# Performance work log

Measured on AMD Instinct MI355X. Metric: run time of the kernel, lower is better.

The kernel has to match this reference:

```python
import jax, jax.numpy as jnp
import numpy as np

H = 16  # num_heads


def setup_inputs() -> dict:
    key = jax.random.key(0)
    ks = jax.random.split(key, 8)
    B, N, C = 16, 4096, 512
    hd = C // H
    sc = lambda k, shape: jax.random.normal(k, shape, jnp.float32) * 0.02
    return {
        "x": jax.random.normal(ks[0], (B, N, C), jnp.float32),
        "Wqkv": sc(ks[1], (C, 3 * C)),
        "bqkv": sc(ks[2], (3 * C,)),
        "pos_enc": jnp.zeros((1, N, C), jnp.float32),
        "dwc_w": sc(ks[3], (hd, 1, 5, 5)),  # OIHW, depthwise: groups = hd
        "dwc_b": sc(ks[4], (hd,)),
        "Wproj": sc(ks[5], (C, C)),
        "bproj": sc(ks[6], (C,)),
    }


def reference(x, Wqkv, bqkv, pos_enc, dwc_w, dwc_b, Wproj, bproj):
    B, N, C = x.shape
    hd = C // H
    # qkv projection
    qkv = x @ Wqkv + bqkv                       # (B, N, 3C)
    q, k, v = jnp.split(qkv, 3, axis=-1)
    k = k + pos_enc
    q = jax.nn.relu(q)
    k = jax.nn.relu(k)

    def heads(t):  # (B, N, C) -> (B*H, N, hd), fp32 as in the torch autocast-off block
        return t.reshape(B, N, H, hd).transpose(0, 2, 1, 3).reshape(B * H, N, hd).astype(jnp.float32)

    q, k, v = heads(q), heads(k), heads(v)
    # normalization z_i = 1 / (q_i . sum_j k_j + eps)
    z = 1.0 / (jnp.einsum('bic,bc->bi', q, k.sum(axis=1)) + 1e-6)   # (B*H, N)
    # kv-first path: i*j*(c+d) > c*d*(i+j) for N=4096, hd=32
    kv = jnp.einsum('bjc,bjd->bcd', k, v)                           # (B*H, hd, hd)
    out = jnp.einsum('bic,bcd->bid', q, kv) * z[..., None]          # (B*H, N, hd)
    # depthwise 5x5 conv on v reshaped to a square feature map
    w = int(N ** 0.5)
    fm = v.transpose(0, 2, 1).reshape(B * H, hd, w, w)
    fm = jax.lax.conv_general_dilated(
        fm, dwc_w, window_strides=(1, 1), padding=[(2, 2), (2, 2)],
        dimension_numbers=('NCHW', 'OIHW', 'NCHW'), feature_group_count=hd)
    fm = fm + dwc_b[None, :, None, None]
    fm = fm.reshape(B * H, hd, N).transpose(0, 2, 1)
    out = out + fm
    # merge heads and project
    out = out.reshape(B, H, N, hd).transpose(0, 2, 1, 3).reshape(B, N, C)
    return out @ Wproj + bproj
```

## Files before the change

### kernel.cpp

```cpp
#include <hip/hip_runtime.h>
#include <stdint.h>

typedef short bf16x8 __attribute__((ext_vector_type(8)));
typedef float f32x4 __attribute__((ext_vector_type(4)));
typedef unsigned short u16x8 __attribute__((ext_vector_type(8)));

__device__ __forceinline__ unsigned short f2bf(float f){
  uint32_t u = __builtin_bit_cast(uint32_t, f);
  u += 0x7FFFu + ((u >> 16) & 1u);
  return (unsigned short)(u >> 16);
}
__device__ __forceinline__ float bf2f(unsigned short h){
  uint32_t u = ((uint32_t)h) << 16;
  return __builtin_bit_cast(float, u);
}
__device__ __forceinline__ float bflo(uint32_t dw){
  return __builtin_bit_cast(float, dw << 16);
}
__device__ __forceinline__ float bfhi(uint32_t dw){
  return __builtin_bit_cast(float, dw & 0xffff0000u);
}

__device__ __forceinline__ void gload_lds16(const void* g, void* l){
  __builtin_amdgcn_global_load_lds(
      (const __attribute__((address_space(1))) uint32_t*)(g),
      (__attribute__((address_space(3))) uint32_t*)(l),
      16, 0, 0);
}

__global__ __launch_bounds__(256) void convert_x_k(const float* __restrict__ x,
                                                   unsigned short* __restrict__ xb){
  size_t i = (size_t)blockIdx.x * 256 + threadIdx.x;
  const float4* p = (const float4*)x + i * 2;
  float4 a = p[0], b = p[1];
  u16x8 o;
  o[0] = f2bf(a.x); o[1] = f2bf(a.y); o[2] = f2bf(a.z); o[3] = f2bf(a.w);
  o[4] = f2bf(b.x); o[5] = f2bf(b.y); o[6] = f2bf(b.z); o[7] = f2bf(b.w);
  *(u16x8*)(xb + i * 8) = o;
}

__global__ __launch_bounds__(256) void transpose_w_k(const float* __restrict__ Wqkv,
                                                     const float* __restrict__ Wproj,
                                                     unsigned short* __restrict__ Wqkvt,
                                                     unsigned short* __restrict__ Wprojt){
  __shared__ unsigned short t[64][68];
  int bid = blockIdx.x;
  const float* src; unsigned short* dst; int c0, j0, sstride, dstride;
  if (bid < 192){
    src = Wqkv;  dst = Wqkvt;  sstride = 1536; dstride = 512;
    c0 = (bid / 24) * 64;  j0 = (bid % 24) * 64;
  } else {
    int e = bid - 192;
    src = Wproj; dst = Wprojt; sstride = 512;  dstride = 512;
    c0 = (e >> 3) * 64;    j0 = (e & 7) * 64;
  }
  int tid = threadIdx.x;
  int rl = tid >> 6;
  int cl = tid & 63;
  #pragma unroll
  for (int i = 0; i < 16; ++i){
    int cr = i * 4 + rl;
    t[cl][cr] = f2bf(src[(size_t)(c0 + cr) * sstride + j0 + cl]);
  }
  __syncthreads();
  #pragma unroll
  for (int i = 0; i < 16; ++i){
    int jr = i * 4 + rl;
    dst[(size_t)(j0 + jr) * dstride + c0 + cl] = t[jr][cl];
  }
}

template<int EPI>
__device__ __forceinline__ void gemm_body(
    const unsigned short* __restrict__ A,
    const unsigned short* __restrict__ Bt,
    const float* __restrict__ bias,
    const float* __restrict__ pos_enc,
    unsigned short* __restrict__ oq,
    unsigned short* __restrict__ ok,
    unsigned short* __restrict__ ov,
    float* __restrict__ op,
    int NTN)
{
  __shared__ unsigned short As[2][256 * 64];
  __shared__ unsigned short Bs[2][256 * 64];
  int tid = threadIdx.x, lane = tid & 63, wid = tid >> 6;
  int nwg = gridDim.x;
  int b0 = blockIdx.x;
  int cpx = nwg >> 3;
  int swz = (b0 & 7) * cpx + (b0 >> 3);
  int tm = swz / NTN, tn = swz - tm * NTN;
  int row0 = tm << 8, col0 = tn << 8;
  int wrow = wid >> 2, wcol = wid & 3;

  f32x4 acc[8][4];
  #pragma unroll
  for (int m = 0; m < 8; ++m)
    #pragma unroll
    for (int n = 0; n < 4; ++n)
      acc[m][n] = (f32x4){0.f, 0.f, 0.f, 0.f};

  auto STAGE = [&](int buf, int kt){
    int k0 = kt * 64;
    #pragma unroll
    for (int it = 0; it < 4; ++it){
      int c = it * 512 + tid;
      int r = c >> 3;
      int scs = ((c & 7) ^ (r & 7)) * 8;
      gload_lds16(A + (size_t)(row0 + r) * 512 + k0 + scs, &As[buf][c * 8]);
    }
    #pragma unroll
    for (int it = 0; it < 4; ++it){
      int c = it * 512 + tid;
      int r = c >> 3;
      int scs = ((c & 7) ^ (r & 7)) * 8;
      gload_lds16(Bt + (size_t)(col0 + r) * 512 + k0 + scs, &Bs[buf][c * 8]);
    }
  };
  auto COMPUTE = [&](int buf){
    bf16x8 bfr[4][2];
    #pragma unroll
    for (int kk = 0; kk < 2; ++kk){
      int kcs = ((kk * 4 + (lane >> 4)) ^ (lane & 7)) * 8;
      #pragma unroll
      for (int n = 0; n < 4; ++n)
        bfr[n][kk] = *(const bf16x8*)&Bs[buf][(wcol * 64 + n * 16 + (lane & 15)) * 64 + kcs];
    }
    __builtin_amdgcn_s_setprio(1);
    #pragma unroll
    for (int kk = 0; kk < 2; ++kk){
      int kcs = ((kk * 4 + (lane >> 4)) ^ (lane & 7)) * 8;
      #pragma unroll
      for (int m = 0; m < 8; ++m){
        bf16x8 af = *(const bf16x8*)&As[buf][(wrow * 128 + m * 16 + (lane & 15)) * 64 + kcs];
        #pragma unroll
        for (int n = 0; n < 4; ++n)
          acc[m][n] = __builtin_amdgcn_mfma_f32_16x16x32_bf16(af, bfr[n][kk], acc[m][n], 0, 0, 0);
      }
    }
    __builtin_amdgcn_s_setprio(0);
  };

  STAGE(0, 0);
  STAGE(1, 1);
  #pragma unroll
  for (int t = 0; t < 8; ++t){
    if (t < 7) asm volatile("s_waitcnt vmcnt(8)" ::: "memory");
    else       asm volatile("s_waitcnt vmcnt(0)" ::: "memory");
    __builtin_amdgcn_s_barrier();
    __builtin_amdgcn_sched_barrier(0);
    COMPUTE(t & 1);
    asm volatile("" ::: "memory");
    __builtin_amdgcn_s_barrier();
    if (t + 2 < 8) STAGE(t & 1, t + 2);
  }

  if constexpr (EPI == 0){
    int part = col0 >> 9;
    int ccb = (col0 & 511) + wcol * 64;
    unsigned short* scr = &As[0][wid * 2048];
    #pragma unroll
    for (int mh = 0; mh < 4; ++mh){
      #pragma unroll
      for (int mm = 0; mm < 2; ++mm){
        int m = mh * 2 + mm;
        #pragma unroll
        for (int n = 0; n < 4; ++n){
          #pragma unroll
          for (int r = 0; r < 4; ++r){
            int lrow = mm * 16 + (lane >> 4) * 4 + r;
            int lcol = n * 16 + (lane & 15);
            float val = acc[m][n][r] + bias[col0 + wcol * 64 + lcol];
            if (part == 0) val = fmaxf(val, 0.f);
            int pch = (lcol >> 3) ^ ((lrow >> 2) & 3);
            scr[lrow * 64 + pch * 8 + (lcol & 7)] = f2bf(val);
          }
        }
      }
      #pragma unroll
      for (int i = 0; i < 4; ++i){
        int idx = i * 64 + lane;
        int r2 = idx >> 3, c2 = idx & 7;
        int pch = c2 ^ ((r2 >> 2) & 3);
        u16x8 vals = *(const u16x8*)&scr[r2 * 64 + pch * 8];
        int grow = row0 + wrow * 128 + mh * 32 + r2;
        int bb = grow >> 12, nn = grow & 4095;
        int cc = ccb + c2 * 8;
        int h = cc >> 5, d = cc & 31;
        size_t dst = ((size_t)((bb << 4) + h) * 4096 + nn) * 32 + d;
        if (part == 1){
          const float4* pe = (const float4*)(pos_enc + (size_t)nn * 512 + cc);
          float4 p0 = pe[0], p1 = pe[1];
          u16x8 o;
          o[0] = f2bf(fmaxf(bf2f(vals[0]) + p0.x, 0.f));
          o[1] = f2bf(fmaxf(bf2f(vals[1]) + p0.y, 0.f));
          o[2] = f2bf(fmaxf(bf2f(vals[2]) + p0.z, 0.f));
          o[3] = f2bf(fmaxf(bf2f(vals[3]) + p0.w, 0.f));
          o[4] = f2bf(fmaxf(bf2f(vals[4]) + p1.x, 0.f));
          o[5] = f2bf(fmaxf(bf2f(vals[5]) + p1.y, 0.f));
          o[6] = f2bf(fmaxf(bf2f(vals[6]) + p1.z, 0.f));
          o[7] = f2bf(fmaxf(bf2f(vals[7]) + p1.w, 0.f));
          *(u16x8*)(ok + dst) = o;
        } else if (part == 0){
          *(u16x8*)(oq + dst) = vals;
        } else {
          *(u16x8*)(ov + dst) = vals;
        }
      }
    }
  } else {
    #pragma unroll
    for (int m = 0; m < 8; ++m){
      #pragma unroll
      for (int n = 0; n < 4; ++n){
        #pragma unroll
        for (int r = 0; r < 4; ++r){
          int rrow = row0 + wrow * 128 + m * 16 + (lane >> 4) * 4 + r;
          int ccol = col0 + wcol * 64 + n * 16 + (lane & 15);
          op[(size_t)rrow * 512 + ccol] = acc[m][n][r] + bias[ccol];
        }
      }
    }
  }
}

__global__ __launch_bounds__(512, 1) void gemm_qkv(
    const unsigned short* __restrict__ A, const unsigned short* __restrict__ Bt,
    const float* __restrict__ bias, const float* __restrict__ pos_enc,
    unsigned short* __restrict__ oq, unsigned short* __restrict__ ok,
    unsigned short* __restrict__ ov, int NTN){
  gemm_body<0>(A, Bt, bias, pos_enc, oq, ok, ov, nullptr, NTN);
}

__global__ __launch_bounds__(512, 1) void gemm_proj(
    const unsigned short* __restrict__ A, const unsigned short* __restrict__ Bt,
    const float* __restrict__ bias, float* __restrict__ op, int NTN){
  gemm_body<1>(A, Bt, bias, nullptr, nullptr, nullptr, nullptr, op, NTN);
}

__global__ __launch_bounds__(256) void transpose_v_k(
    const unsigned short* __restrict__ vbuf, uint32_t* __restrict__ vp){
  __shared__ uint32_t tile[256][17];
  int chunk = blockIdx.x & 15;
  int bh    = blockIdx.x >> 4;
  int tid = threadIdx.x;
  const unsigned short* src = vbuf + (size_t)bh * 131072 + (size_t)chunk * 256 * 32;
  #pragma unroll
  for (int i = 0; i < 4; ++i){
    u16x8 vv = *(const u16x8*)(src + tid * 32 + i * 8);
    uint4 q = __builtin_bit_cast(uint4, vv);
    tile[tid][i * 4 + 0] = q.x;
    tile[tid][i * 4 + 1] = q.y;
    tile[tid][i * 4 + 2] = q.z;
    tile[tid][i * 4 + 3] = q.w;
  }
  __syncthreads();
  uint32_t* dstb = vp + (size_t)bh * 65536 + chunk * 256;
  #pragma unroll
  for (int i = 0; i < 16; ++i){
    dstb[i * 4096 + tid] = tile[tid][i];
  }
}

__global__ __launch_bounds__(256, 2) void attn_k3(
    const unsigned short* __restrict__ qbuf,
    const uint32_t* __restrict__ vp,
    const float* __restrict__ kvb,
    const float* __restrict__ ksb,
    const float* __restrict__ dwc_w,
    const float* __restrict__ dwc_b,
    unsigned short* __restrict__ attn)
{
  int band = blockIdx.x;
  int bh   = blockIdx.y;
  int tid = threadIdx.x, lane = tid & 63, w = tid >> 6;
  __shared__ uint32_t outs32[1024][18];
  unsigned short* outs = (unsigned short*)outs32;
  __shared__ float zs[1024];
  __shared__ float ksum_s[32];

  const unsigned short* qb = qbuf + (size_t)bh * 4096 * 32 + (size_t)band * 1024 * 32;
  const uint32_t* vpb = vp + (size_t)bh * 65536;

  if (tid < 32) ksum_s[tid] = ksb[bh * 32 + tid];
  __syncthreads();

  for (int p = 0; p < 4; ++p){
    int t = p * 256 + tid;
    float zd = 0.f;
    #pragma unroll
    for (int pp = 0; pp < 4; ++pp){
      u16x8 qq = *(const u16x8*)(qb + (size_t)t * 32 + pp * 8);
      #pragma unroll
      for (int i = 0; i < 8; ++i) zd += bf2f(qq[i]) * ksum_s[pp * 8 + i];
    }
    zs[t] = 1.f / (zd + 1e-6f);
  }

  bf16x8 bfr[2];
  #pragma unroll
  for (int nc = 0; nc < 2; ++nc){
    bf16x8 t8;
    #pragma unroll
    for (int j = 0; j < 8; ++j){
      int c = (lane >> 4) * 8 + j;
      int d = nc * 16 + (lane & 15);
      t8[j] = (short)f2bf(kvb[bh * 1024 + c * 32 + d]);
    }
    bfr[nc] = t8;
  }
  __syncthreads();

  for (int p = 0; p < 4; ++p){
    f32x4 acc[4][2];
    #pragma unroll
    for (int m = 0; m < 4; ++m){ acc[m][0] = (f32x4){0.f,0.f,0.f,0.f}; acc[m][1] = (f32x4){0.f,0.f,0.f,0.f}; }
    #pragma unroll
    for (int m = 0; m < 4; ++m){
      int row = p * 256 + w * 64 + m * 16 + (lane & 15);
      bf16x8 af = *(const bf16x8*)(qb + (size_t)row * 32 + (lane >> 4) * 8);
      acc[m][0] = __builtin_amdgcn_mfma_f32_16x16x32_bf16(af, bfr[0], acc[m][0], 0, 0, 0);
      acc[m][1] = __builtin_amdgcn_mfma_f32_16x16x32_bf16(af, bfr[1], acc[m][1], 0, 0, 0);
    }
    #pragma unroll
    for (int m = 0; m < 4; ++m)
      #pragma unroll
      for (int nc = 0; nc < 2; ++nc)
        #pragma unroll
        for (int r = 0; r < 4; ++r){
          int lrow = p * 256 + w * 64 + m * 16 + (lane >> 4) * 4 + r;
          int col = nc * 16 + (lane & 15);
          outs[lrow * 36 + col] = f2bf(acc[m][nc][r] * zs[lrow]);
        }
  }
  __syncthreads();

  int x = lane;
  int y0 = band * 16;
  int xm2 = lane - 2, xm1 = lane - 1, xp1 = lane + 1, xp2 = lane + 2;

  for (int pair = 0; pair < 4; ++pair){
    int dbase = w * 8 + pair * 2;
    int pr = w * 4 + pair;
    float w0[25], w1[25];
    #pragma unroll
    for (int j = 0; j < 25; ++j){
      w0[j] = dwc_w[dbase * 25 + j];
      w1[j] = dwc_w[(dbase + 1) * 25 + j];
    }
    float cb0 = dwc_b[dbase], cb1 = dwc_b[dbase + 1];

    uint32_t rowd[20];
    #pragma unroll
    for (int il = 0; il < 20; ++il){
      int yi = y0 - 2 + il;
      rowd[il] = (yi >= 0 && yi < 64)
        ? vpb[pr * 4096 + yi * 64 + x] : 0u;
    }

    float a0[5], a1[5];
    #pragma unroll
    for (int il = 0; il < 20; ++il){
      uint32_t d0 = rowd[il];
      uint32_t dm2 = (uint32_t)__shfl((int)d0, xm2); if (lane < 2)  dm2 = 0;
      uint32_t dm1 = (uint32_t)__shfl((int)d0, xm1); if (lane < 1)  dm1 = 0;
      uint32_t dp1 = (uint32_t)__shfl((int)d0, xp1); if (lane > 62) dp1 = 0;
      uint32_t dp2 = (uint32_t)__shfl((int)d0, xp2); if (lane > 61) dp2 = 0;
      float f0[5], f1[5];
      f0[0] = bflo(dm2); f1[0] = bfhi(dm2);
      f0[1] = bflo(dm1); f1[1] = bfhi(dm1);
      f0[2] = bflo(d0);  f1[2] = bfhi(d0);
      f0[3] = bflo(dp1); f1[3] = bfhi(dp1);
      f0[4] = bflo(dp2); f1[4] = bfhi(dp2);
      #pragma unroll
      for (int ky = 0; ky < 5; ++ky){
        int ol = il - ky;
        if (ol < 0 || ol > 15) continue;
        int s = ol % 5;
        if (ky == 0){
          a0[s] = w0[0] * f0[0];
          a1[s] = w1[0] * f1[0];
          #pragma unroll
          for (int kx = 1; kx < 5; ++kx){
            a0[s] += w0[kx] * f0[kx];
            a1[s] += w1[kx] * f1[kx];
          }
        } else {
          #pragma unroll
          for (int kx = 0; kx < 5; ++kx){
            a0[s] += w0[ky * 5 + kx] * f0[kx];
            a1[s] += w1[ky * 5 + kx] * f1[kx];
          }
        }
      }
      if (il >= 4){
        int ol = il - 4;
        int s = ol % 5;
        int ltok = ol * 64 + x;
        uint32_t ov = outs32[ltok][pr];
        float o0 = bflo(ov) + a0[s] + cb0;
        float o1 = bfhi(ov) + a1[s] + cb1;
        outs32[ltok][pr] = ((uint32_t)f2bf(o1) << 16) | (uint32_t)f2bf(o0);
      }
    }
  }
  __syncthreads();

  int b = bh >> 4, h = bh & 15;
  size_t gbase = ((size_t)b * 4096 + (size_t)band * 1024) * 512 + h * 32;
  #pragma unroll
  for (int it = 0; it < 32; ++it){
    int idx = it * 256 + tid;
    int token = idx >> 3, sub = idx & 7;
    uint2 vv = *(const uint2*)&outs32[token][sub * 2];
    *(uint2*)(attn + gbase + (size_t)token * 512 + sub * 4) = vv;
  }
}

__global__ __launch_bounds__(256) void kv_k(const unsigned short* __restrict__ kbuf,
                                            const unsigned short* __restrict__ vbuf,
                                            float* __restrict__ kvb,
                                            float* __restrict__ ksb){
  int bh  = blockIdx.x >> 2;
  int seg = blockIdx.x & 3;
  __shared__ float ks[64][36];
  __shared__ float vs[64][36];
  __shared__ float red[4][64][16];
  __shared__ float ksred[4][8][4];
  int tid = threadIdx.x;
  int g = tid >> 6, gi = tid & 63;
  int c0 = (gi >> 3) * 4, d0 = (gi & 7) * 4;
  float acc[4][4] = {};
  float ksacc[4] = {0.f, 0.f, 0.f, 0.f};
  const unsigned short* kb = kbuf + (size_t)bh * 4096 * 32 + (size_t)seg * 1024 * 32;
  const unsigned short* vb = vbuf + (size_t)bh * 4096 * 32 + (size_t)seg * 1024 * 32;
  int er = tid >> 2;
  int ec = (tid & 3) * 8;
  for (int t = 0; t < 16; ++t){
    __syncthreads();
    u16x8 kk8 = *(const u16x8*)(kb + ((size_t)t * 64 + er) * 32 + ec);
    u16x8 vv8 = *(const u16x8*)(vb + ((size_t)t * 64 + er) * 32 + ec);
    #pragma unroll
    for (int i = 0; i < 8; ++i){ ks[er][ec + i] = bf2f(kk8[i]); vs[er][ec + i] = bf2f(vv8[i]); }
    __syncthreads();
    for (int nn = g; nn < 64; nn += 4){
      f32x4 k4 = *(const f32x4*)&ks[nn][c0];
      f32x4 v4 = *(const f32x4*)&vs[nn][d0];
      #pragma unroll
      for (int i = 0; i < 4; ++i)
        #pragma unroll
        for (int j = 0; j < 4; ++j)
          acc[i][j] += k4[i] * v4[j];
      if ((gi & 7) == 0){
        #pragma unroll
        for (int i = 0; i < 4; ++i) ksacc[i] += k4[i];
      }
    }
  }
  __syncthreads();
  #pragma unroll
  for (int i = 0; i < 4; ++i)
    #pragma unroll
    for (int j = 0; j < 4; ++j)
      red[g][gi][i * 4 + j] = acc[i][j];
  if ((gi & 7) == 0){
    #pragma unroll
    for (int i = 0; i < 4; ++i) ksred[g][gi >> 3][i] = ksacc[i];
  }
  __syncthreads();
  for (int s = tid; s < 1024; s += 256){
    int gi2 = s >> 4, e = s & 15;
    float sum = red[0][gi2][e] + red[1][gi2][e] + red[2][gi2][e] + red[3][gi2][e];
    int c = (gi2 >> 3) * 4 + (e >> 2), d = (gi2 & 7) * 4 + (e & 3);
    atomicAdd(&kvb[bh * 1024 + c * 32 + d], sum);
  }
  if (tid < 32){
    float s = ksred[0][tid >> 2][tid & 3] + ksred[1][tid >> 2][tid & 3]
            + ksred[2][tid >> 2][tid & 3] + ksred[3][tid >> 2][tid & 3];
    atomicAdd(&ksb[bh * 32 + tid], s);
  }
}

extern "C" void kernel_launch(void* const* d_in, const int* in_sizes, int n_in,
                              void* d_out, int out_size, void* d_ws, size_t ws_size,
                              hipStream_t stream) {
  const float* x       = (const float*)d_in[0];
  const float* Wqkv    = (const float*)d_in[1];
  const float* bqkv    = (const float*)d_in[2];
  const float* pos_enc = (const float*)d_in[3];
  const float* dwc_w   = (const float*)d_in[4];
  const float* dwc_b   = (const float*)d_in[5];
  const float* Wproj   = (const float*)d_in[6];
  const float* bproj   = (const float*)d_in[7];
  float* out = (float*)d_out;
  char* ws = (char*)d_ws;

  const size_t off_xb    = 0;
  const size_t off_wqkvt = 67108864;
  const size_t off_wprojt= 68681728;
  const size_t off_q     = 69206016;
  const size_t off_k     = 136314880;
  const size_t off_v     = 203423744;
  const size_t off_kv    = 270532608;
  const size_t off_ksum  = 271581184;
  const size_t needed    = 271613952;
  if (ws_size < needed) return;

  unsigned short* xb     = (unsigned short*)(ws + off_xb);
  unsigned short* wqkvt  = (unsigned short*)(ws + off_wqkvt);
  unsigned short* wprojt = (unsigned short*)(ws + off_wprojt);
  unsigned short* qb     = (unsigned short*)(ws + off_q);
  unsigned short* kb     = (unsigned short*)(ws + off_k);
  unsigned short* vb     = (unsigned short*)(ws + off_v);
  float* kvb = (float*)(ws + off_kv);
  float* ksb = (float*)(ws + off_ksum);
  unsigned short* attn = kb;
  uint32_t* vp = (uint32_t*)(ws + off_xb);

  convert_x_k<<<16384, 256, 0, stream>>>(x, xb);
  transpose_w_k<<<256, 256, 0, stream>>>(Wqkv, Wproj, wqkvt, wprojt);
  gemm_qkv<<<1536, 512, 0, stream>>>(xb, wqkvt, bqkv, pos_enc, qb, kb, vb, 6);
  (void)hipMemsetAsync(kvb, 0, (size_t)(256 * 1024 + 256 * 32) * sizeof(float), stream);
  transpose_v_k<<<4096, 256, 0, stream>>>(vb, vp);
  kv_k<<<1024, 256, 0, stream>>>(kb, vb, kvb, ksb);
  attn_k3<<<dim3(4, 256), 256, 0, stream>>>(qb, vp, kvb, ksb, dwc_w, dwc_b, attn);
  gemm_proj<<<512, 512, 0, stream>>>(attn, wprojt, bproj, out, 2);
}
```

Baseline: 400.4 us.

## Use smaller single-buffered QKV GEMM tiles and fuse V transpose into kv kernel

The QKV GEMM becomes its own kernel with 256x128 tiles, single-buffered LDS and launch bounds allowing two workgroups per CU, doubling the grid. This trades the old double-buffered 256x256 pipeline for higher occupancy. The separate transpose_v_k kernel is removed. kv_k now writes the packed, transposed V layout from the tile it already stages in LDS, saving one full read pass over V and one launch. The simpler GEMM loop has no explicit prefetch, so global-load latency may be less hidden.

```diff
diff --git a/kernel.cpp b/kernel.cpp
--- a/kernel.cpp
+++ b/kernel.cpp
@@ -70,8 +70,7 @@
   }
 }
 
-template<int EPI>
-__device__ __forceinline__ void gemm_body(
+__global__ __launch_bounds__(512, 2) void gemm_qkv(
     const unsigned short* __restrict__ A,
     const unsigned short* __restrict__ Bt,
     const float* __restrict__ bias,
@@ -79,6 +78,120 @@
     unsigned short* __restrict__ oq,
     unsigned short* __restrict__ ok,
     unsigned short* __restrict__ ov,
+    int NTN)
+{
+  __shared__ unsigned short As[256 * 64];
+  __shared__ unsigned short Bs[128 * 64];
+  int tid = threadIdx.x, lane = tid & 63, wid = tid >> 6;
+  int nwg = gridDim.x;
+  int b0 = blockIdx.x;
+  int cpx = nwg >> 3;
+  int swz = (b0 & 7) * cpx + (b0 >> 3);
+  int tm = swz / NTN, tn = swz - tm * NTN;
+  int row0 = tm << 8, col0 = tn << 7;
+  int wr = wid >> 1, wc = wid & 1;
+
+  f32x4 acc[4][4];
+  #pragma unroll
+  for (int m = 0; m < 4; ++m)
+    #pragma unroll
+    for (int n = 0; n < 4; ++n)
+      acc[m][n] = (f32x4){0.f, 0.f, 0.f, 0.f};
+
+  for (int kt = 0; kt < 8; ++kt){
+    int k0 = kt * 64;
+    #pragma unroll
+    for (int it = 0; it < 4; ++it){
+      int c = it * 512 + tid;
+      int r = c >> 3;
+      int scs = ((c & 7) ^ (r & 7)) * 8;
+      gload_lds16(A + (size_t)(row0 + r) * 512 + k0 + scs, &As[c * 8]);
+    }
+    #pragma unroll
+    for (int it = 0; it < 2; ++it){
+      int c = it * 512 + tid;
+      int r = c >> 3;
+      int scs = ((c & 7) ^ (r & 7)) * 8;
+      gload_lds16(Bt + (size_t)(col0 + r) * 512 + k0 + scs, &Bs[c * 8]);
+    }
+    __syncthreads();
+    #pragma unroll
+    for (int kk = 0; kk < 2; ++kk){
+      bf16x8 af[4], bfr[4];
+      int kcs = ((kk * 4 + (lane >> 4)) ^ (lane & 7)) * 8;
+      #pragma unroll
+      for (int m = 0; m < 4; ++m)
+        af[m] = *(const bf16x8*)&As[(wr * 64 + m * 16 + (lane & 15)) * 64 + kcs];
+      #pragma unroll
+      for (int n = 0; n < 4; ++n)
+        bfr[n] = *(const bf16x8*)&Bs[(wc * 64 + n * 16 + (lane & 15)) * 64 + kcs];
+      #pragma unroll
+      for (int m = 0; m < 4; ++m)
+        #pragma unroll
+        for (int n = 0; n < 4; ++n)
+          acc[m][n] = __builtin_amdgcn_mfma_f32_16x16x32_bf16(af[m], bfr[n], acc[m][n], 0, 0, 0);
+    }
+    __syncthreads();
+  }
+
+  int part = col0 >> 9;
+  int ccb = (col0 & 511) + wc * 64;
+  unsigned short* scr = &As[wid * 2048];
+  #pragma unroll
+  for (int mh = 0; mh < 2; ++mh){
+    #pragma unroll
+    for (int mm = 0; mm < 2; ++mm){
+      int m = mh * 2 + mm;
+      #pragma unroll
+      for (int n = 0; n < 4; ++n){
+        #pragma unroll
+        for (int r = 0; r < 4; ++r){
+          int lrow = mm * 16 + (lane >> 4) * 4 + r;
+          int lcol = n * 16 + (lane & 15);
+          float val = acc[m][n][r] + bias[col0 + wc * 64 + lcol];
+          if (part == 0) val = fmaxf(val, 0.f);
+          int pch = (lcol >> 3) ^ ((lrow >> 2) & 3);
+          scr[lrow * 64 + pch * 8 + (lcol & 7)] = f2bf(val);
+        }
+      }
+    }
+    #pragma unroll
+    for (int i = 0; i < 4; ++i){
+      int idx = i * 64 + lane;
+      int r2 = idx >> 3, c2 = idx & 7;
+      int pch = c2 ^ ((r2 >> 2) & 3);
+      u16x8 vals = *(const u16x8*)&scr[r2 * 64 + pch * 8];
+      int grow = row0 + wr * 64 + mh * 32 + r2;
+      int bb = grow >> 12, nn = grow & 4095;
+      int cc = ccb + c2 * 8;
+      int h = cc >> 5, d = cc & 31;
+      size_t dst = ((size_t)((bb << 4) + h) * 4096 + nn) * 32 + d;
+      if (part == 1){
+        const float4* pe = (const float4*)(pos_enc + (size_t)nn * 512 + cc);
+        float4 p0 = pe[0], p1 = pe[1];
+        u16x8 o;
+        o[0] = f2bf(fmaxf(bf2f(vals[0]) + p0.x, 0.f));
+        o[1] = f2bf(fmaxf(bf2f(vals[1]) + p0.y, 0.f));
+        o[2] = f2bf(fmaxf(bf2f(vals[2]) + p0.z, 0.f));
+        o[3] = f2bf(fmaxf(bf2f(vals[3]) + p0.w, 0.f));
+        o[4] = f2bf(fmaxf(bf2f(vals[4]) + p1.x, 0.f));
+        o[5] = f2bf(fmaxf(bf2f(vals[5]) + p1.y, 0.f));
+        o[6] = f2bf(fmaxf(bf2f(vals[6]) + p1.z, 0.f));
+        o[7] = f2bf(fmaxf(bf2f(vals[7]) + p1.w, 0.f));
+        *(u16x8*)(ok + dst) = o;
+      } else if (part == 0){
+        *(u16x8*)(oq + dst) = vals;
+      } else {
+        *(u16x8*)(ov + dst) = vals;
+      }
+    }
+  }
+}
+
+__global__ __launch_bounds__(512, 1) void gemm_proj(
+    const unsigned short* __restrict__ A,
+    const unsigned short* __restrict__ Bt,
+    const float* __restrict__ bias,
     float* __restrict__ op,
     int NTN)
 {
@@ -155,110 +268,91 @@
     if (t + 2 < 8) STAGE(t & 1, t + 2);
   }
 
-  if constexpr (EPI == 0){
-    int part = col0 >> 9;
-    int ccb = (col0 & 511) + wcol * 64;
-    unsigned short* scr = &As[0][wid * 2048];
-    #pragma unroll
-    for (int mh = 0; mh < 4; ++mh){
-      #pragma unroll
-      for (int mm = 0; mm < 2; ++mm){
-        int m = mh * 2 + mm;
+  #pragma unroll
+  for (int m = 0; m < 8; ++m){
+    #pragma unroll
+    for (int n = 0; n < 4; ++n){
+      #pragma unroll
+      for (int r = 0; r < 4; ++r){
+        int rrow = row0 + wrow * 128 + m * 16 + (lane >> 4) * 4 + r;
+        int ccol = col0 + wcol * 64 + n * 16 + (lane & 15);
+        op[(size_t)rrow * 512 + ccol] = acc[m][n][r] + bias[ccol];
+      }
+    }
+  }
+}
+
+__global__ __launch_bounds__(256) void kv_k(const unsigned short* __restrict__ kbuf,
+                                            const unsigned short* __restrict__ vbuf,
+                                            float* __restrict__ kvb,
+                                            float* __restrict__ ksb,
+                                            uint32_t* __restrict__ vp){
+  int bh  = blockIdx.x >> 2;
+  int seg = blockIdx.x & 3;
+  __shared__ float ks[64][36];
+  __shared__ float vs[64][36];
+  __shared__ float red[4][64][16];
+  __shared__ float ksred[4][8][4];
+  int tid = threadIdx.x;
+  int g = tid >> 6, gi = tid & 63;
+  int c0 = (gi >> 3) * 4, d0 = (gi & 7) * 4;
+  float acc[4][4] = {};
+  float ksacc[4] = {0.f, 0.f, 0.f, 0.f};
+  const unsigned short* kb = kbuf + (size_t)bh * 4096 * 32 + (size_t)seg * 1024 * 32;
+  const unsigned short* vb = vbuf + (size_t)bh * 4096 * 32 + (size_t)seg * 1024 * 32;
+  uint32_t* vpb = vp + (size_t)bh * 65536 + seg * 1024;
+  int er = tid >> 2;
+  int ec = (tid & 3) * 8;
+  for (int t = 0; t < 16; ++t){
+    __syncthreads();
+    u16x8 kk8 = *(const u16x8*)(kb + ((size_t)t * 64 + er) * 32 + ec);
+    u16x8 vv8 = *(const u16x8*)(vb + ((size_t)t * 64 + er) * 32 + ec);
+    #pragma unroll
+    for (int i = 0; i < 8; ++i){ ks[er][ec + i] = bf2f(kk8[i]); vs[er][ec + i] = bf2f(vv8[i]); }
+    __syncthreads();
+    #pragma unroll
+    for (int i = 0; i < 4; ++i){
+      int idx = i * 256 + tid;
+      int pr = idx >> 6, tok = idx & 63;
+      uint32_t pk = ((uint32_t)f2bf(vs[tok][pr * 2 + 1]) << 16)
+                  |  (uint32_t)f2bf(vs[tok][pr * 2]);
+      vpb[pr * 4096 + t * 64 + tok] = pk;
+    }
+    for (int nn = g; nn < 64; nn += 4){
+      f32x4 k4 = *(const f32x4*)&ks[nn][c0];
+      f32x4 v4 = *(const f32x4*)&vs[nn][d0];
+      #pragma unroll
+      for (int i = 0; i < 4; ++i)
         #pragma unroll
-        for (int n = 0; n < 4; ++n){
-          #pragma unroll
-          for (int r = 0; r < 4; ++r){
-            int lrow = mm * 16 + (lane >> 4) * 4 + r;
-            int lcol = n * 16 + (lane & 15);
-            float val = acc[m][n][r] + bias[col0 + wcol * 64 + lcol];
-            if (part == 0) val = fmaxf(val, 0.f);
-            int pch = (lcol >> 3) ^ ((lrow >> 2) & 3);
-            scr[lrow * 64 + pch * 8 + (lcol & 7)] = f2bf(val);
-          }
-        }
-      }
-      #pragma unroll
-      for (int i = 0; i < 4; ++i){
-        int idx = i * 64 + lane;
-        int r2 = idx >> 3, c2 = idx & 7;
-        int pch = c2 ^ ((r2 >> 2) & 3);
-        u16x8 vals = *(const u16x8*)&scr[r2 * 64 + pch * 8];
-        int grow = row0 + wrow * 128 + mh * 32 + r2;
-        int bb = grow >> 12, nn = grow & 4095;
-        int cc = ccb + c2 * 8;
-        int h = cc >> 5, d = cc & 31;
-        size_t dst = ((size_t)((bb << 4) + h) * 4096 + nn) * 32 + d;
-        if (part == 1){
-          const float4* pe = (const float4*)(pos_enc + (size_t)nn * 512 + cc);
-          float4 p0 = pe[0], p1 = pe[1];
-          u16x8 o;
-          o[0] = f2bf(fmaxf(bf2f(vals[0]) + p0.x, 0.f));
-          o[1] = f2bf(fmaxf(bf2f(vals[1]) + p0.y, 0.f));
-          o[2] = f2bf(fmaxf(bf2f(vals[2]) + p0.z, 0.f));
-          o[3] = f2bf(fmaxf(bf2f(vals[3]) + p0.w, 0.f));
-          o[4] = f2bf(fmaxf(bf2f(vals[4]) + p1.x, 0.f));
-          o[5] = f2bf(fmaxf(bf2f(vals[5]) + p1.y, 0.f));
-          o[6] = f2bf(fmaxf(bf2f(vals[6]) + p1.z, 0.f));
-          o[7] = f2bf(fmaxf(bf2f(vals[7]) + p1.w, 0.f));
-          *(u16x8*)(ok + dst) = o;
-        } else if (part == 0){
-          *(u16x8*)(oq + dst) = vals;
-        } else {
-          *(u16x8*)(ov + dst) = vals;
-        }
-      }
-    }
-  } else {
-    #pragma unroll
-    for (int m = 0; m < 8; ++m){
-      #pragma unroll
-      for (int n = 0; n < 4; ++n){
+        for (int j = 0; j < 4; ++j)
+          acc[i][j] += k4[i] * v4[j];
+      if ((gi & 7) == 0){
         #pragma unroll
-        for (int r = 0; r < 4; ++r){
-          int rrow = row0 + wrow * 128 + m * 16 + (lane >> 4) * 4 + r;
-          int ccol = col0 + wcol * 64 + n * 16 + (lane & 15);
-          op[(size_t)rrow * 512 + ccol] = acc[m][n][r] + bias[ccol];
-        }
-      }
-    }
-  }
-}
-
-__global__ __launch_bounds__(512, 1) void gemm_qkv(
-    const unsigned short* __restrict__ A, const unsigned short* __restrict__ Bt,
-    const float* __restrict__ bias, const float* __restrict__ pos_enc,
-    unsigned short* __restrict__ oq, unsigned short* __restrict__ ok,
-    unsigned short* __restrict__ ov, int NTN){
-  gemm_body<0>(A, Bt, bias, pos_enc, oq, ok, ov, nullptr, NTN);
-}
-
-__global__ __launch_bounds__(512, 1) void gemm_proj(
-    const unsigned short* __restrict__ A, const unsigned short* __restrict__ Bt,
-    const float* __restrict__ bias, float* __restrict__ op, int NTN){
-  gemm_body<1>(A, Bt, bias, nullptr, nullptr, nullptr, nullptr, op, NTN);
-}
-
-__global__ __launch_bounds__(256) void transpose_v_k(
-    const unsigned short* __restrict__ vbuf, uint32_t* __restrict__ vp){
-  __shared__ uint32_t tile[256][17];
-  int chunk = blockIdx.x & 15;
-  int bh    = blockIdx.x >> 4;
-  int tid = threadIdx.x;
-  const unsigned short* src = vbuf + (size_t)bh * 131072 + (size_t)chunk * 256 * 32;
-  #pragma unroll
-  for (int i = 0; i < 4; ++i){
-    u16x8 vv = *(const u16x8*)(src + tid * 32 + i * 8);
-    uint4 q = __builtin_bit_cast(uint4, vv);
-    tile[tid][i * 4 + 0] = q.x;
-    tile[tid][i * 4 + 1] = q.y;
-    tile[tid][i * 4 + 2] = q.z;
-    tile[tid][i * 4 + 3] = q.w;
-  }
-  __syncthreads();
-  uint32_t* dstb = vp + (size_t)bh * 65536 + chunk * 256;
-  #pragma unroll
-  for (int i = 0; i < 16; ++i){
-    dstb[i * 4096 + tid] = tile[tid][i];
+        for (int i = 0; i < 4; ++i) ksacc[i] += k4[i];
+      }
+    }
+  }
+  __syncthreads();
+  #pragma unroll
+  for (int i = 0; i < 4; ++i)
+    #pragma unroll
+    for (int j = 0; j < 4; ++j)
+      red[g][gi][i * 4 + j] = acc[i][j];
+  if ((gi & 7) == 0){
+    #pragma unroll
+    for (int i = 0; i < 4; ++i) ksred[g][gi >> 3][i] = ksacc[i];
+  }
+  __syncthreads();
+  for (int s = tid; s < 1024; s += 256){
+    int gi2 = s >> 4, e = s & 15;
+    float sum = red[0][gi2][e] + red[1][gi2][e] + red[2][gi2][e] + red[3][gi2][e];
+    int c = (gi2 >> 3) * 4 + (e >> 2), d = (gi2 & 7) * 4 + (e & 3);
+    atomicAdd(&kvb[bh * 1024 + c * 32 + d], sum);
+  }
+  if (tid < 32){
+    float s = ksred[0][tid >> 2][tid & 3] + ksred[1][tid >> 2][tid & 3]
+            + ksred[2][tid >> 2][tid & 3] + ksred[3][tid >> 2][tid & 3];
+    atomicAdd(&ksb[bh * 32 + tid], s);
   }
 }
 
@@ -417,70 +511,6 @@
   }
 }
 
-__global__ __launch_bounds__(256) void kv_k(const unsigned short* __restrict__ kbuf,
-                                            const unsigned short* __restrict__ vbuf,
-                                            float* __restrict__ kvb,
-                                            float* __restrict__ ksb){
-  int bh  = blockIdx.x >> 2;
-  int seg = blockIdx.x & 3;
-  __shared__ float ks[64][36];
-  __shared__ float vs[64][36];
-  __shared__ float red[4][64][16];
-  __shared__ float ksred[4][8][4];
-  int tid = threadIdx.x;
-  int g = tid >> 6, gi = tid & 63;
-  int c0 = (gi >> 3) * 4, d0 = (gi & 7) * 4;
-  float acc[4][4] = {};
-  float ksacc[4] = {0.f, 0.f, 0.f, 0.f};
-  const unsigned short* kb = kbuf + (size_t)bh * 4096 * 32 + (size_t)seg * 1024 * 32;
-  const unsigned short* vb = vbuf + (size_t)bh * 4096 * 32 + (size_t)seg * 1024 * 32;
-  int er = tid >> 2;
-  int ec = (tid & 3) * 8;
-  for (int t = 0; t < 16; ++t){
-    __syncthreads();
-    u16x8 kk8 = *(const u16x8*)(kb + ((size_t)t * 64 + er) * 32 + ec);
-    u16x8 vv8 = *(const u16x8*)(vb + ((size_t)t * 64 + er) * 32 + ec);
-    #pragma unroll
-    for (int i = 0; i < 8; ++i){ ks[er][ec + i] = bf2f(kk8[i]); vs[er][ec + i] = bf2f(vv8[i]); }
-    __syncthreads();
-    for (int nn = g; nn < 64; nn += 4){
-      f32x4 k4 = *(const f32x4*)&ks[nn][c0];
-      f32x4 v4 = *(const f32x4*)&vs[nn][d0];
-      #pragma unroll
-      for (int i = 0; i < 4; ++i)
-        #pragma unroll
-        for (int j = 0; j < 4; ++j)
-          acc[i][j] += k4[i] * v4[j];
-      if ((gi & 7) == 0){
-        #pragma unroll
-        for (int i = 0; i < 4; ++i) ksacc[i] += k4[i];
-      }
-    }
-  }
-  __syncthreads();
-  #pragma unroll
-  for (int i = 0; i < 4; ++i)
-    #pragma unroll
-    for (int j = 0; j < 4; ++j)
-      red[g][gi][i * 4 + j] = acc[i][j];
-  if ((gi & 7) == 0){
-    #pragma unroll
-    for (int i = 0; i < 4; ++i) ksred[g][gi >> 3][i] = ksacc[i];
-  }
-  __syncthreads();
-  for (int s = tid; s < 1024; s += 256){
-    int gi2 = s >> 4, e = s & 15;
-    float sum = red[0][gi2][e] + red[1][gi2][e] + red[2][gi2][e] + red[3][gi2][e];
-    int c = (gi2 >> 3) * 4 + (e >> 2), d = (gi2 & 7) * 4 + (e & 3);
-    atomicAdd(&kvb[bh * 1024 + c * 32 + d], sum);
-  }
-  if (tid < 32){
-    float s = ksred[0][tid >> 2][tid & 3] + ksred[1][tid >> 2][tid & 3]
-            + ksred[2][tid >> 2][tid & 3] + ksred[3][tid >> 2][tid & 3];
-    atomicAdd(&ksb[bh * 32 + tid], s);
-  }
-}
-
 extern "C" void kernel_launch(void* const* d_in, const int* in_sizes, int n_in,
                               void* d_out, int out_size, void* d_ws, size_t ws_size,
                               hipStream_t stream) {
@@ -519,10 +549,9 @@
 
   convert_x_k<<<16384, 256, 0, stream>>>(x, xb);
   transpose_w_k<<<256, 256, 0, stream>>>(Wqkv, Wproj, wqkvt, wprojt);
-  gemm_qkv<<<1536, 512, 0, stream>>>(xb, wqkvt, bqkv, pos_enc, qb, kb, vb, 6);
+  gemm_qkv<<<3072, 512, 0, stream>>>(xb, wqkvt, bqkv, pos_enc, qb, kb, vb, 12);
   (void)hipMemsetAsync(kvb, 0, (size_t)(256 * 1024 + 256 * 32) * sizeof(float), stream);
-  transpose_v_k<<<4096, 256, 0, stream>>>(vb, vp);
-  kv_k<<<1024, 256, 0, stream>>>(kb, vb, kvb, ksb);
+  kv_k<<<1024, 256, 0, stream>>>(kb, vb, kvb, ksb, vp);
   attn_k3<<<dim3(4, 256), 256, 0, stream>>>(qb, vp, kvb, ksb, dwc_w, dwc_b, attn);
   gemm_proj<<<512, 512, 0, stream>>>(attn, wprojt, bproj, out, 2);
 }
```

Measured after the change: 390.0 us. 2.6% less time.
